# Performance work log

Measured on AMD Instinct MI355X. Metric: run time of the kernel, lower is better.

The kernel has to match this reference:

```python
import jax, jax.numpy as jnp
import numpy as np

N = 100000
E = 3200000
IN_DIM = 256
HID = 64
NC = 32
K1 = 2  # conv1 propagation steps
EPS = 1e-5


def setup_inputs() -> dict:
    key = jax.random.key(0)
    ks = jax.random.split(key, 8)
    x = jax.random.normal(ks[0], (N, IN_DIM), dtype=jnp.float32)
    src = jax.random.randint(ks[1], (E,), 0, N)
    dst = jax.random.randint(ks[2], (E,), 0, N)
    W1 = jax.random.normal(ks[3], (IN_DIM, HID), dtype=jnp.float32) / np.sqrt(IN_DIM)
    b1 = jnp.zeros((HID,), dtype=jnp.float32)
    gamma = jnp.ones((HID,), dtype=jnp.float32)
    beta = jnp.zeros((HID,), dtype=jnp.float32)
    W2 = jax.random.normal(ks[4], (HID, NC), dtype=jnp.float32) / np.sqrt(HID)
    b2 = jnp.zeros((NC,), dtype=jnp.float32)
    return {"x": x, "src": src, "dst": dst, "W1": W1, "b1": b1,
            "gamma": gamma, "beta": beta, "W2": W2, "b2": b2}


def _gcn_norm(src, dst, n):
    # deg includes self loop (add_self_loops=True): deg[i] = 1 + in-degree
    deg = jax.ops.segment_sum(jnp.ones_like(src, dtype=jnp.float32), dst, num_segments=n) + 1.0
    dinv = jax.lax.rsqrt(deg)
    w_edge = dinv[src] * dinv[dst]      # [E] normalized edge weights
    w_self = dinv * dinv                # [N] self-loop weights (1/deg)
    return w_edge, w_self


def _propagate(h, src, dst, w_edge, w_self, n):
    # out = D^-1/2 (A+I) D^-1/2 h  via gather-scale-scatter
    msg = w_edge[:, None] * h[src]
    agg = jax.ops.segment_sum(msg, dst, num_segments=n)
    return agg + w_self[:, None] * h


def reference(x, src, dst, W1, b1, gamma, beta, W2, b2):
    n = x.shape[0]
    w_edge, w_self = _gcn_norm(src, dst, n)
    # conv1: K-step propagation then linear
    h = x
    for _ in range(K1):
        h = _propagate(h, src, dst, w_edge, w_self, n)
    h = h @ W1 + b1
    # batchnorm (training-mode batch stats over nodes, biased variance)
    mean = jnp.mean(h, axis=0)
    var = jnp.mean(jnp.square(h - mean), axis=0)
    h = (h - mean) * jax.lax.rsqrt(var + EPS) * gamma + beta
    h = jax.nn.selu(h)
    # dropout p=0.0 -> identity
    # conv2: 1-step propagation then linear
    h = _propagate(h, src, dst, w_edge, w_self, n)
    h = h @ W2 + b2
    return jax.nn.log_softmax(h, axis=1)
```

## Files before the change

kernel.cpp:

```cpp
#include <hip/hip_runtime.h>
#include <hip/hip_fp16.h>

#define NN 100000
#define EE 3200000
#define NB 256
#define NPB 391
#define BCAP 13568
#define NBLK_A 1024
#define CHUNK_A (EE / NBLK_A)

#define OFF_AF   0UL
#define OFF_AH   25600000UL
#define OFF_BH   38400000UL
#define OFF_CSR  51200000UL
#define OFF_RP   64000000UL
#define OFF_DINV 64400384UL
#define OFF_SEG  64800768UL
#define OFF_BASE 64808960UL
#define OFF_BN   64813056UL
#define OFF_SS   64813568UL

typedef __attribute__((ext_vector_type(8))) short bf16x8;
typedef __attribute__((ext_vector_type(4))) float f32x4;

__global__ __launch_bounds__(256) void passA(const int* __restrict__ src, const int* __restrict__ dst,
                                             int* __restrict__ segcnt, unsigned* __restrict__ buf) {
    __shared__ int hist[NB];
    __shared__ int curl[NB];
    int t = threadIdx.x;
    hist[t] = 0;
    __syncthreads();
    int beg = blockIdx.x * CHUNK_A, end = beg + CHUNK_A;
    for (int i = beg + t; i < end; i += 256)
        atomicAdd(&hist[dst[i] / NPB], 1);
    __syncthreads();
    int h = hist[t];
    int r = atomicAdd(&segcnt[t], h);
    curl[t] = t * BCAP + r;
    __syncthreads();
    for (int i = beg + t; i < end; i += 256) {
        int d = dst[i];
        int k = d / NPB;
        int dl = d - k * NPB;
        int p = atomicAdd(&curl[k], 1);
        if (p < (k + 1) * BCAP)
            buf[p] = ((unsigned)dl << 17) | (unsigned)src[i];
    }
}

__global__ __launch_bounds__(256) void scan_buckets(const int* __restrict__ segcnt,
                                                    int* __restrict__ base, int* __restrict__ rp) {
    __shared__ int s[256];
    int t = threadIdx.x;
    int tot = min(segcnt[t], BCAP);
    s[t] = tot;
    __syncthreads();
    for (int off = 1; off < 256; off <<= 1) {
        int v = (t >= off) ? s[t - off] : 0;
        __syncthreads();
        s[t] += v;
        __syncthreads();
    }
    base[t] = s[t] - tot;
    if (t == 255) { base[256] = s[255]; rp[NN] = s[255]; }
}

__global__ __launch_bounds__(256) void passB(const unsigned* __restrict__ buf,
                                             const int* __restrict__ segcnt,
                                             const int* __restrict__ base,
                                             int* __restrict__ rp, float* __restrict__ dinv,
                                             int* __restrict__ csr) {
    __shared__ unsigned ebuf[BCAP];
    __shared__ int deg_l[NPB];
    __shared__ int off_l[NPB];
    __shared__ int s[256];
    __shared__ int tot0;
    int b = blockIdx.x, t = threadIdx.x;
    int nb = min(segcnt[b], BCAP);
    for (int i = t; i < NPB; i += 256) deg_l[i] = 0;
    const unsigned* sp = buf + (size_t)b * BCAP;
    for (int j = t; j < nb; j += 256) ebuf[j] = sp[j];
    __syncthreads();
    for (int j = t; j < nb; j += 256) atomicAdd(&deg_l[ebuf[j] >> 17], 1);
    __syncthreads();
    int d0 = deg_l[t];
    s[t] = d0;
    __syncthreads();
    for (int off = 1; off < 256; off <<= 1) {
        int v = (t >= off) ? s[t - off] : 0;
        __syncthreads();
        s[t] += v;
        __syncthreads();
    }
    off_l[t] = s[t] - d0;
    if (t == 255) tot0 = s[255];
    __syncthreads();
    int i1 = 256 + t;
    int d1 = (i1 < NPB) ? deg_l[i1] : 0;
    s[t] = d1;
    __syncthreads();
    for (int off = 1; off < 256; off <<= 1) {
        int v = (t >= off) ? s[t - off] : 0;
        __syncthreads();
        s[t] += v;
        __syncthreads();
    }
    if (i1 < NPB) off_l[i1] = tot0 + s[t] - d1;
    __syncthreads();
    int nodebase = b * NPB;
    int cbase = base[b];
    for (int i = t; i < NPB; i += 256) {
        int node = nodebase + i;
        if (node < NN) {
            rp[node] = cbase + off_l[i];
            dinv[node] = rsqrtf((float)deg_l[i] + 1.0f);
        }
    }
    __syncthreads();
    for (int j = t; j < nb; j += 256) {
        unsigned e = ebuf[j];
        int p = atomicAdd(&off_l[e >> 17], 1);
        csr[cbase + p] = (int)(e & 0x1FFFFu);
    }
}

__global__ __launch_bounds__(256) void wprep(const float* __restrict__ W1, short* __restrict__ wf) {
    int e = blockIdx.x * 256 + threadIdx.x;
    if (e >= 16384) return;
    int j = e & 7, lane = (e >> 3) & 63, nt = (e >> 9) & 3, ks = e >> 11;
    int k = ks * 32 + (lane >> 4) * 8 + j;
    int col = nt * 16 + (lane & 15);
    float w = W1[k * 64 + col];
    unsigned b = __float_as_uint(w);
    short hi = (short)(b >> 16);
    float hf = __uint_as_float(b & 0xFFFF0000u);
    float lo = w - hf;
    short lov = (short)(__float_as_uint(lo) >> 16);
    wf[((size_t)(ks * 8 + nt * 2 + 0) * 64 + lane) * 8 + j] = hi;
    wf[((size_t)(ks * 8 + nt * 2 + 1) * 64 + lane) * 8 + j] = lov;
}

__global__ __launch_bounds__(256) void gemm1(const float* __restrict__ x, const short* __restrict__ wf,
                                             const float* __restrict__ dinv, __half* __restrict__ Ah) {
    int wid = threadIdx.x >> 6, lane = threadIdx.x & 63;
    int g = blockIdx.x * 4 + wid;
    if (g >= NN / 16) return;
    int lrow = g * 16 + (lane & 15);
    int kgrp = (lane >> 4) * 8;
    const float* xp = x + (size_t)lrow * 256 + kgrp;
    f32x4 acc[4];
    #pragma unroll
    for (int nt = 0; nt < 4; ++nt) acc[nt] = (f32x4){0.f, 0.f, 0.f, 0.f};
    for (int ks = 0; ks < 8; ++ks) {
        float4 f0 = *(const float4*)(xp + ks * 32);
        float4 f1 = *(const float4*)(xp + ks * 32 + 4);
        bf16x8 a_hi, a_lo;
        const float* fp = &f0.x;
        #pragma unroll
        for (int j = 0; j < 8; ++j) {
            float f = (j < 4) ? fp[j] : (&f1.x)[j - 4];
            unsigned b = __float_as_uint(f);
            a_hi[j] = (short)(b >> 16);
            float lo = f - __uint_as_float(b & 0xFFFF0000u);
            a_lo[j] = (short)(__float_as_uint(lo) >> 16);
        }
        const short* wfk = wf + (size_t)(ks * 8) * 64 * 8;
        #pragma unroll
        for (int nt = 0; nt < 4; ++nt) {
            bf16x8 b_hi = *(const bf16x8*)(wfk + ((nt * 2 + 0) * 64 + lane) * 8);
            bf16x8 b_lo = *(const bf16x8*)(wfk + ((nt * 2 + 1) * 64 + lane) * 8);
            acc[nt] = __builtin_amdgcn_mfma_f32_16x16x32_bf16(a_hi, b_hi, acc[nt], 0, 0, 0);
            acc[nt] = __builtin_amdgcn_mfma_f32_16x16x32_bf16(a_hi, b_lo, acc[nt], 0, 0, 0);
            acc[nt] = __builtin_amdgcn_mfma_f32_16x16x32_bf16(a_lo, b_hi, acc[nt], 0, 0, 0);
        }
    }
    int mb = (lane >> 4) * 4;
    #pragma unroll
    for (int reg = 0; reg < 4; ++reg) {
        int row = g * 16 + mb + reg;
        float dv = dinv[row];
        #pragma unroll
        for (int nt = 0; nt < 4; ++nt)
            Ah[(size_t)row * 64 + nt * 16 + (lane & 15)] = __float2half(acc[nt][reg] * dv);
    }
}

template <int P>
__global__ __launch_bounds__(256) void agg64h(const __half* __restrict__ h, __half* __restrict__ outp,
                                              const int* __restrict__ rp, const int* __restrict__ csr,
                                              const float* __restrict__ dinv) {
    int lane = threadIdx.x & 63;
    int node = (blockIdx.x << 2) + (threadIdx.x >> 6);
    if (node >= NN) return;
    int hid = lane >> 5;
    int c2 = (lane & 31) * 2;
    float dd = dinv[node];
    float ax = 0.f, ay = 0.f, bx = 0.f, by = 0.f;
    if (hid == 0) {
        __half2 sv = *(const __half2*)(h + (size_t)node * 64 + c2);
        ax = __half2float(sv.x); ay = __half2float(sv.y);
    }
    int beg = rp[node], end = rp[node + 1];
    for (int j0 = beg; j0 < end; j0 += 64) {
        int m = end - j0; if (m > 64) m = 64;
        int s = csr[j0 + (lane < m ? lane : 0)];
        int j = 0;
        for (; j + 15 < m; j += 16) {
            int i0 = __shfl(s, j + hid);
            int i1 = __shfl(s, j + 2 + hid);
            int i2 = __shfl(s, j + 4 + hid);
            int i3 = __shfl(s, j + 6 + hid);
            int i4 = __shfl(s, j + 8 + hid);
            int i5 = __shfl(s, j + 10 + hid);
            int i6 = __shfl(s, j + 12 + hid);
            int i7 = __shfl(s, j + 14 + hid);
            __half2 v0 = *(const __half2*)(h + (size_t)i0 * 64 + c2);
            __half2 v1 = *(const __half2*)(h + (size_t)i1 * 64 + c2);
            __half2 v2 = *(const __half2*)(h + (size_t)i2 * 64 + c2);
            __half2 v3 = *(const __half2*)(h + (size_t)i3 * 64 + c2);
            __half2 v4 = *(const __half2*)(h + (size_t)i4 * 64 + c2);
            __half2 v5 = *(const __half2*)(h + (size_t)i5 * 64 + c2);
            __half2 v6 = *(const __half2*)(h + (size_t)i6 * 64 + c2);
            __half2 v7 = *(const __half2*)(h + (size_t)i7 * 64 + c2);
            ax += __half2float(v0.x) + __half2float(v2.x);
            ay += __half2float(v0.y) + __half2float(v2.y);
            bx += __half2float(v1.x) + __half2float(v3.x);
            by += __half2float(v1.y) + __half2float(v3.y);
            ax += __half2float(v4.x) + __half2float(v6.x);
            ay += __half2float(v4.y) + __half2float(v6.y);
            bx += __half2float(v5.x) + __half2float(v7.x);
            by += __half2float(v5.y) + __half2float(v7.y);
        }
        for (; j + 7 < m; j += 8) {
            int i0 = __shfl(s, j + hid);
            int i1 = __shfl(s, j + 2 + hid);
            int i2 = __shfl(s, j + 4 + hid);
            int i3 = __shfl(s, j + 6 + hid);
            __half2 v0 = *(const __half2*)(h + (size_t)i0 * 64 + c2);
            __half2 v1 = *(const __half2*)(h + (size_t)i1 * 64 + c2);
            __half2 v2 = *(const __half2*)(h + (size_t)i2 * 64 + c2);
            __half2 v3 = *(const __half2*)(h + (size_t)i3 * 64 + c2);
            ax += __half2float(v0.x) + __half2float(v2.x);
            ay += __half2float(v0.y) + __half2float(v2.y);
            bx += __half2float(v1.x) + __half2float(v3.x);
            by += __half2float(v1.y) + __half2float(v3.y);
        }
        for (; j < m; j += 2) {
            int idx = j + hid;
            int cidx = idx < m ? idx : m - 1;
            int sj = __shfl(s, cidx);
            if (idx < m) {
                __half2 v = *(const __half2*)(h + (size_t)sj * 64 + c2);
                ax += __half2float(v.x); ay += __half2float(v.y);
            }
        }
    }
    float sx = ax + bx, sy = ay + by;
    sx += __shfl(sx, lane ^ 32);
    sy += __shfl(sy, lane ^ 32);
    if (hid == 0) {
        float w = (P == 2) ? dd * dd : dd;
        __half2 o;
        o.x = __float2half(sx * w); o.y = __float2half(sy * w);
        *(__half2*)(outp + (size_t)node * 64 + c2) = o;
    }
}

__global__ __launch_bounds__(256) void agg32f(const __half* __restrict__ U, float* __restrict__ outp,
                                              const int* __restrict__ rp, const int* __restrict__ csr,
                                              const float* __restrict__ dinv, const float* __restrict__ b2) {
    int lane = threadIdx.x & 63;
    int node = (blockIdx.x << 2) + (threadIdx.x >> 6);
    if (node >= NN) return;
    int gid = lane >> 4;
    int c2 = (lane & 15) * 2;
    float dd = dinv[node];
    float ax = 0.f, ay = 0.f;
    if (gid == 0) {
        __half2 sv = *(const __half2*)(U + (size_t)node * 32 + c2);
        ax = __half2float(sv.x); ay = __half2float(sv.y);
    }
    int beg = rp[node], end = rp[node + 1];
    for (int j0 = beg; j0 < end; j0 += 64) {
        int m = end - j0; if (m > 64) m = 64;
        int s = csr[j0 + (lane < m ? lane : 0)];
        int j = 0;
        for (; j + 15 < m; j += 16) {
            int i0 = __shfl(s, j + gid);
            int i1 = __shfl(s, j + 4 + gid);
            int i2 = __shfl(s, j + 8 + gid);
            int i3 = __shfl(s, j + 12 + gid);
            __half2 v0 = *(const __half2*)(U + (size_t)i0 * 32 + c2);
            __half2 v1 = *(const __half2*)(U + (size_t)i1 * 32 + c2);
            __half2 v2 = *(const __half2*)(U + (size_t)i2 * 32 + c2);
            __half2 v3 = *(const __half2*)(U + (size_t)i3 * 32 + c2);
            ax += __half2float(v0.x) + __half2float(v1.x) + __half2float(v2.x) + __half2float(v3.x);
            ay += __half2float(v0.y) + __half2float(v1.y) + __half2float(v2.y) + __half2float(v3.y);
        }
        for (; j + 7 < m; j += 8) {
            int i0 = __shfl(s, j + gid);
            int i1 = __shfl(s, j + 4 + gid);
            __half2 v0 = *(const __half2*)(U + (size_t)i0 * 32 + c2);
            __half2 v1 = *(const __half2*)(U + (size_t)i1 * 32 + c2);
            ax += __half2float(v0.x) + __half2float(v1.x);
            ay += __half2float(v0.y) + __half2float(v1.y);
        }
        for (; j < m; j += 4) {
            int idx = j + gid;
            int cidx = idx < m ? idx : m - 1;
            int sj = __shfl(s, cidx);
            if (idx < m) {
                __half2 v = *(const __half2*)(U + (size_t)sj * 32 + c2);
                ax += __half2float(v.x); ay += __half2float(v.y);
            }
        }
    }
    ax += __shfl(ax, lane ^ 16); ay += __shfl(ay, lane ^ 16);
    ax += __shfl(ax, lane ^ 32); ay += __shfl(ay, lane ^ 32);
    float v0 = ax * dd + b2[c2];
    float v1 = ay * dd + b2[c2 + 1];
    float mx = fmaxf(v0, v1);
    mx = fmaxf(mx, __shfl_xor(mx, 1));
    mx = fmaxf(mx, __shfl_xor(mx, 2));
    mx = fmaxf(mx, __shfl_xor(mx, 4));
    mx = fmaxf(mx, __shfl_xor(mx, 8));
    float sum = __expf(v0 - mx) + __expf(v1 - mx);
    sum += __shfl_xor(sum, 1);
    sum += __shfl_xor(sum, 2);
    sum += __shfl_xor(sum, 4);
    sum += __shfl_xor(sum, 8);
    if (gid == 0) {
        float ls = __logf(sum);
        *(float2*)(outp + (size_t)node * 32 + c2) = make_float2(v0 - mx - ls, v1 - mx - ls);
    }
}

__global__ __launch_bounds__(256) void bn_stats(const __half* __restrict__ A, float* __restrict__ bn) {
    int t = threadIdx.x;
    int c = t & 63, rg = t >> 6;
    float s = 0.f, sq = 0.f;
    for (int r = blockIdx.x * 4 + rg; r < NN; r += gridDim.x * 4) {
        float v = __half2float(A[(size_t)r * 64 + c]);
        s += v; sq += v * v;
    }
    __shared__ float ls[256], lq[256];
    ls[t] = s; lq[t] = sq;
    __syncthreads();
    if (t < 64) {
        float S = ls[t] + ls[t + 64] + ls[t + 128] + ls[t + 192];
        float Q = lq[t] + lq[t + 64] + lq[t + 128] + lq[t + 192];
        atomicAdd(&bn[t], S);
        atomicAdd(&bn[64 + t], Q);
    }
}

__global__ void bn_final(const float* __restrict__ bn, const float* __restrict__ gamma,
                         const float* __restrict__ beta, float* __restrict__ ss) {
    int c = threadIdx.x;
    float mean = bn[c] / (float)NN;
    float var = bn[64 + c] / (float)NN - mean * mean;
    float sc = gamma[c] * rsqrtf(var + 1e-5f);
    ss[c] = sc;
    ss[64 + c] = beta[c] - mean * sc;
}

__global__ __launch_bounds__(256) void gemm2(const __half* __restrict__ A, const float* __restrict__ W2,
                                             const float* __restrict__ ss, const float* __restrict__ dinv,
                                             __half* __restrict__ U) {
    __shared__ float w2s[64 * 32];
    __shared__ float sc[64], sh[64];
    for (int i = threadIdx.x; i < 512; i += 256)
        ((float4*)w2s)[i] = ((const float4*)W2)[i];
    if (threadIdx.x < 64) {
        sc[threadIdx.x] = ss[threadIdx.x];
        sh[threadIdx.x] = ss[64 + threadIdx.x];
    }
    __syncthreads();
    const float SELU_S = 1.0507009873554805f;
    const float SELU_AS = 1.7580993408473766f;
    int lane = threadIdx.x & 31, grp = threadIdx.x >> 5;
    int node = blockIdx.x * 8 + grp;
    if (node >= NN) return;
    const __half* Ar = A + (size_t)node * 64;
    float v0 = __half2float(Ar[lane]);
    float v1 = __half2float(Ar[lane + 32]);
    v0 = v0 * sc[lane] + sh[lane];
    v1 = v1 * sc[lane + 32] + sh[lane + 32];
    v0 = v0 > 0.f ? SELU_S * v0 : SELU_AS * (__expf(v0) - 1.0f);
    v1 = v1 > 0.f ? SELU_S * v1 : SELU_AS * (__expf(v1) - 1.0f);
    float acc = 0.f;
    #pragma unroll
    for (int j = 0; j < 32; ++j) {
        acc += __shfl(v0, j, 32) * w2s[j * 32 + lane];
        acc += __shfl(v1, j, 32) * w2s[(j + 32) * 32 + lane];
    }
    U[(size_t)node * 32 + lane] = __float2half(dinv[node] * acc);
}

extern "C" void kernel_launch(void* const* d_in, const int* in_sizes, int n_in,
                              void* d_out, int out_size, void* d_ws, size_t ws_size,
                              hipStream_t stream) {
    const float* x     = (const float*)d_in[0];
    const int*   src   = (const int*)d_in[1];
    const int*   dst   = (const int*)d_in[2];
    const float* W1    = (const float*)d_in[3];
    const float* gamma = (const float*)d_in[5];
    const float* beta  = (const float*)d_in[6];
    const float* W2    = (const float*)d_in[7];
    const float* b2    = (const float*)d_in[8];
    float* out = (float*)d_out;

    char* ws = (char*)d_ws;
    __half*   Af   = (__half*)(ws + OFF_AF);
    unsigned* bbuf = (unsigned*)(ws + OFF_AF);
    __half*   Ah   = (__half*)(ws + OFF_AH);
    __half*   Bh   = (__half*)(ws + OFF_BH);
    short*    wf   = (short*)(ws + OFF_BH);
    __half*   Uh   = (__half*)(ws + OFF_BH);
    int*      csr  = (int*)(ws + OFF_CSR);
    int*      rp   = (int*)(ws + OFF_RP);
    float*    dinv = (float*)(ws + OFF_DINV);
    int*      seg  = (int*)(ws + OFF_SEG);
    int*      base = (int*)(ws + OFF_BASE);
    float*    bn   = (float*)(ws + OFF_BN);
    float*    ssb  = (float*)(ws + OFF_SS);

    hipMemsetAsync(seg, 0, NB * sizeof(int), stream);
    hipMemsetAsync(bn, 0, 128 * sizeof(float), stream);

    wprep<<<64, 256, 0, stream>>>(W1, wf);

    passA<<<NBLK_A, 256, 0, stream>>>(src, dst, seg, bbuf);
    scan_buckets<<<1, 256, 0, stream>>>(seg, base, rp);
    passB<<<NB, 256, 0, stream>>>(bbuf, seg, base, rp, dinv, csr);

    gemm1<<<(NN / 16 + 3) / 4, 256, 0, stream>>>(x, wf, dinv, Ah);
    agg64h<2><<<NN / 4, 256, 0, stream>>>(Ah, Bh, rp, csr, dinv);
    agg64h<1><<<NN / 4, 256, 0, stream>>>(Bh, Af, rp, csr, dinv);

    bn_stats<<<1024, 256, 0, stream>>>(Af, bn);
    bn_final<<<1, 64, 0, stream>>>(bn, gamma, beta, ssb);

    gemm2<<<NN / 8, 256, 0, stream>>>(Af, W2, ssb, dinv, Uh);
    agg32f<<<NN / 4, 256, 0, stream>>>(Uh, out, rp, csr, dinv, b2);
}
```

Measured before the change: 357.8 us.

## Replace global-atomic bucket scatter with block-local sort and column scans

The CSR build now has each of 512 blocks sort its edge chunk by bucket in shared memory and write it out contiguously, with per-block counts and offsets. Column and base scans replace the global atomic counters. passB2 then gathers each bucket's segments from every block using 512 threads. This removes scattered global writes and global atomics, at the cost of an extra kernel launch, per-block count/offset arrays, and many small segmented reads in passB2.

```diff
diff --git a/kernel.cpp b/kernel.cpp
--- a/kernel.cpp
+++ b/kernel.cpp
@@ -6,12 +6,15 @@
 #define NB 256
 #define NPB 391
 #define BCAP 13568
-#define NBLK_A 1024
+#define NBLK_A 512
 #define CHUNK_A (EE / NBLK_A)
 
 #define OFF_AF   0UL
 #define OFF_AH   25600000UL
 #define OFF_BH   38400000UL
+#define OFF_CNT  (OFF_BH + 65536UL)
+#define OFF_LOC  (OFF_CNT + 524288UL)
+#define OFF_P    (OFF_LOC + 524288UL)
 #define OFF_CSR  51200000UL
 #define OFF_RP   64000000UL
 #define OFF_DINV 64400384UL
@@ -23,93 +26,116 @@
 typedef __attribute__((ext_vector_type(8))) short bf16x8;
 typedef __attribute__((ext_vector_type(4))) float f32x4;
 
-__global__ __launch_bounds__(256) void passA(const int* __restrict__ src, const int* __restrict__ dst,
-                                             int* __restrict__ segcnt, unsigned* __restrict__ buf) {
-    __shared__ int hist[NB];
-    __shared__ int curl[NB];
-    int t = threadIdx.x;
+__global__ __launch_bounds__(256) void passA2(const int* __restrict__ src, const int* __restrict__ dst,
+                                              int* __restrict__ cnt, int* __restrict__ loc,
+                                              unsigned* __restrict__ gbuf) {
+    __shared__ unsigned ebuf[CHUNK_A];
+    __shared__ int hist[NB], cur[NB], sc[NB];
+    int t = threadIdx.x, b = blockIdx.x;
     hist[t] = 0;
     __syncthreads();
-    int beg = blockIdx.x * CHUNK_A, end = beg + CHUNK_A;
-    for (int i = beg + t; i < end; i += 256)
-        atomicAdd(&hist[dst[i] / NPB], 1);
+    int beg = b * CHUNK_A;
+    for (int i = t; i < CHUNK_A; i += 256)
+        atomicAdd(&hist[dst[beg + i] / NPB], 1);
     __syncthreads();
     int h = hist[t];
-    int r = atomicAdd(&segcnt[t], h);
-    curl[t] = t * BCAP + r;
-    __syncthreads();
-    for (int i = beg + t; i < end; i += 256) {
-        int d = dst[i];
+    sc[t] = h;
+    __syncthreads();
+    for (int off = 1; off < 256; off <<= 1) {
+        int v = (t >= off) ? sc[t - off] : 0;
+        __syncthreads();
+        sc[t] += v;
+        __syncthreads();
+    }
+    int ex = sc[t] - h;
+    cur[t] = ex;
+    loc[b * NB + t] = ex;
+    cnt[b * NB + t] = h;
+    __syncthreads();
+    for (int i = t; i < CHUNK_A; i += 256) {
+        int d = dst[beg + i];
         int k = d / NPB;
         int dl = d - k * NPB;
-        int p = atomicAdd(&curl[k], 1);
-        if (p < (k + 1) * BCAP)
-            buf[p] = ((unsigned)dl << 17) | (unsigned)src[i];
-    }
-}
-
-__global__ __launch_bounds__(256) void scan_buckets(const int* __restrict__ segcnt,
-                                                    int* __restrict__ base, int* __restrict__ rp) {
+        int p = atomicAdd(&cur[k], 1);
+        ebuf[p] = ((unsigned)dl << 17) | (unsigned)src[beg + i];
+    }
+    __syncthreads();
+    for (int i = t; i < CHUNK_A; i += 256)
+        gbuf[beg + i] = ebuf[i];
+}
+
+__global__ __launch_bounds__(512) void colscan(const int* __restrict__ cnt, int* __restrict__ P,
+                                               int* __restrict__ total) {
+    __shared__ int s[512];
+    int k = blockIdx.x, t = threadIdx.x;
+    int v = cnt[t * NB + k];
+    s[t] = v;
+    __syncthreads();
+    for (int off = 1; off < 512; off <<= 1) {
+        int u = (t >= off) ? s[t - off] : 0;
+        __syncthreads();
+        s[t] += u;
+        __syncthreads();
+    }
+    P[t * NB + k] = s[t] - v;
+    if (t == 511) total[k] = s[511];
+}
+
+__global__ __launch_bounds__(256) void basescan(const int* __restrict__ total, int* __restrict__ base,
+                                                int* __restrict__ rp) {
     __shared__ int s[256];
     int t = threadIdx.x;
-    int tot = min(segcnt[t], BCAP);
-    s[t] = tot;
+    int v = total[t];
+    s[t] = v;
     __syncthreads();
     for (int off = 1; off < 256; off <<= 1) {
-        int v = (t >= off) ? s[t - off] : 0;
-        __syncthreads();
-        s[t] += v;
-        __syncthreads();
-    }
-    base[t] = s[t] - tot;
+        int u = (t >= off) ? s[t - off] : 0;
+        __syncthreads();
+        s[t] += u;
+        __syncthreads();
+    }
+    base[t] = s[t] - v;
     if (t == 255) { base[256] = s[255]; rp[NN] = s[255]; }
 }
 
-__global__ __launch_bounds__(256) void passB(const unsigned* __restrict__ buf,
-                                             const int* __restrict__ segcnt,
-                                             const int* __restrict__ base,
-                                             int* __restrict__ rp, float* __restrict__ dinv,
-                                             int* __restrict__ csr) {
+__global__ __launch_bounds__(512) void passB2(const unsigned* __restrict__ gbuf,
+                                              const int* __restrict__ cnt, const int* __restrict__ loc,
+                                              const int* __restrict__ P, const int* __restrict__ total,
+                                              const int* __restrict__ base,
+                                              int* __restrict__ rp, float* __restrict__ dinv,
+                                              int* __restrict__ csr) {
     __shared__ unsigned ebuf[BCAP];
     __shared__ int deg_l[NPB];
     __shared__ int off_l[NPB];
-    __shared__ int s[256];
-    __shared__ int tot0;
-    int b = blockIdx.x, t = threadIdx.x;
-    int nb = min(segcnt[b], BCAP);
-    for (int i = t; i < NPB; i += 256) deg_l[i] = 0;
-    const unsigned* sp = buf + (size_t)b * BCAP;
-    for (int j = t; j < nb; j += 256) ebuf[j] = sp[j];
-    __syncthreads();
-    for (int j = t; j < nb; j += 256) atomicAdd(&deg_l[ebuf[j] >> 17], 1);
-    __syncthreads();
-    int d0 = deg_l[t];
+    __shared__ int s[512];
+    int k = blockIdx.x, t = threadIdx.x;
+    int nb = min(total[k], BCAP);
+    for (int i = t; i < NPB; i += 512) deg_l[i] = 0;
+    int wid = t >> 6, lane = t & 63;
+    for (int b = wid; b < NBLK_A; b += 8) {
+        int n = cnt[b * NB + k];
+        int so = b * CHUNK_A + loc[b * NB + k];
+        int dofs = P[b * NB + k];
+        for (int e = lane; e < n; e += 64)
+            if (dofs + e < BCAP) ebuf[dofs + e] = gbuf[so + e];
+    }
+    __syncthreads();
+    for (int j = t; j < nb; j += 512) atomicAdd(&deg_l[ebuf[j] >> 17], 1);
+    __syncthreads();
+    int d0 = (t < NPB) ? deg_l[t] : 0;
     s[t] = d0;
     __syncthreads();
-    for (int off = 1; off < 256; off <<= 1) {
+    for (int off = 1; off < 512; off <<= 1) {
         int v = (t >= off) ? s[t - off] : 0;
         __syncthreads();
         s[t] += v;
         __syncthreads();
     }
-    off_l[t] = s[t] - d0;
-    if (t == 255) tot0 = s[255];
-    __syncthreads();
-    int i1 = 256 + t;
-    int d1 = (i1 < NPB) ? deg_l[i1] : 0;
-    s[t] = d1;
-    __syncthreads();
-    for (int off = 1; off < 256; off <<= 1) {
-        int v = (t >= off) ? s[t - off] : 0;
-        __syncthreads();
-        s[t] += v;
-        __syncthreads();
-    }
-    if (i1 < NPB) off_l[i1] = tot0 + s[t] - d1;
-    __syncthreads();
-    int nodebase = b * NPB;
-    int cbase = base[b];
-    for (int i = t; i < NPB; i += 256) {
+    if (t < NPB) off_l[t] = s[t] - d0;
+    __syncthreads();
+    int nodebase = k * NPB;
+    int cbase = base[k];
+    for (int i = t; i < NPB; i += 512) {
         int node = nodebase + i;
         if (node < NN) {
             rp[node] = cbase + off_l[i];
@@ -117,7 +143,7 @@
         }
     }
     __syncthreads();
-    for (int j = t; j < nb; j += 256) {
+    for (int j = t; j < nb; j += 512) {
         unsigned e = ebuf[j];
         int p = atomicAdd(&off_l[e >> 17], 1);
         csr[cbase + p] = (int)(e & 0x1FFFFu);
@@ -412,27 +438,30 @@
 
     char* ws = (char*)d_ws;
     __half*   Af   = (__half*)(ws + OFF_AF);
-    unsigned* bbuf = (unsigned*)(ws + OFF_AF);
+    unsigned* gbuf = (unsigned*)(ws + OFF_AF);
     __half*   Ah   = (__half*)(ws + OFF_AH);
     __half*   Bh   = (__half*)(ws + OFF_BH);
     short*    wf   = (short*)(ws + OFF_BH);
     __half*   Uh   = (__half*)(ws + OFF_BH);
+    int*      cnt  = (int*)(ws + OFF_CNT);
+    int*      loc  = (int*)(ws + OFF_LOC);
+    int*      Pm   = (int*)(ws + OFF_P);
     int*      csr  = (int*)(ws + OFF_CSR);
     int*      rp   = (int*)(ws + OFF_RP);
     float*    dinv = (float*)(ws + OFF_DINV);
-    int*      seg  = (int*)(ws + OFF_SEG);
+    int*      tot  = (int*)(ws + OFF_SEG);
     int*      base = (int*)(ws + OFF_BASE);
     float*    bn   = (float*)(ws + OFF_BN);
     float*    ssb  = (float*)(ws + OFF_SS);
 
-    hipMemsetAsync(seg, 0, NB * sizeof(int), stream);
     hipMemsetAsync(bn, 0, 128 * sizeof(float), stream);
 
     wprep<<<64, 256, 0, stream>>>(W1, wf);
 
-    passA<<<NBLK_A, 256, 0, stream>>>(src, dst, seg, bbuf);
-    scan_buckets<<<1, 256, 0, stream>>>(seg, base, rp);
-    passB<<<NB, 256, 0, stream>>>(bbuf, seg, base, rp, dinv, csr);
+    passA2<<<NBLK_A, 256, 0, stream>>>(src, dst, cnt, loc, gbuf);
+    colscan<<<NB, 512, 0, stream>>>(cnt, Pm, tot);
+    basescan<<<1, 256, 0, stream>>>(tot, base, rp);
+    passB2<<<NB, 512, 0, stream>>>(gbuf, cnt, loc, Pm, tot, base, rp, dinv, csr);
 
     gemm1<<<(NN / 16 + 3) / 4, 256, 0, stream>>>(x, wf, dinv, Ah);
     agg64h<2><<<NN / 4, 256, 0, stream>>>(Ah, Bh, rp, csr, dinv);
```

Measured after the change: 388.7 us. +8.6%, slower.
